# Kernel optimization log

Hardware: AMD Instinct MI355X
Metric: run time of the kernel (lower is better)

## Reference

```python
import math
import jax, jax.numpy as jnp
import numpy as np

HEADS = 8
SCALE_BASE = 512.0
GN_EPS = 1e-5


def _gammas(heads):
    # 1 - exp(linspace(log(1/32), log(1/512), heads))
    return 1.0 - np.exp(np.linspace(math.log(1.0 / 32.0), math.log(1.0 / 512.0), heads))


def _xpos(x, downscale):
    # x: (N, S, d), d even. Faithful to torchscale XPOS with scale_base=512.
    N, S, d = x.shape
    half = d // 2
    scale = (jnp.arange(0, d, 2, dtype=jnp.float32) + 0.4 * d) / (1.4 * d)        # (half,)
    pos = jnp.arange(S, dtype=jnp.float32)
    sc = scale[None, :] ** (pos / SCALE_BASE)[:, None]                             # (S, half)
    inv_freq = 1.0 / (10000.0 ** (jnp.arange(half, dtype=jnp.float32) / half))
    sinusoid = pos[:, None] * inv_freq[None, :]                                    # (S, half)
    sin, cos = jnp.sin(sinusoid), jnp.cos(sinusoid)
    if downscale:
        sc = 1.0 / sc
    # duplicate_interleave == repeat each column twice adjacently
    sin_s = jnp.repeat(sin * sc, 2, axis=-1)                                       # (S, d)
    cos_s = jnp.repeat(cos * sc, 2, axis=-1)
    x1, x2 = x[..., ::2], x[..., 1::2]
    rot = jnp.stack((-x2, x1), axis=-1).reshape(x.shape)                           # rotate_every_two
    return x * cos_s + rot * sin_s


def setup_inputs() -> dict:
    key = jax.random.key(0)
    ks = jax.random.split(key, 6)
    B, S, H = 2, 2048, 1024
    h = HEADS
    d = H // h
    X = jax.random.normal(ks[0], (B, S, H), dtype=jnp.float32)
    # per-head projections, torch init: randn(d, d) / d
    W_Q = jax.random.normal(ks[1], (h, d, d), dtype=jnp.float32) / d
    W_K = jax.random.normal(ks[2], (h, d, d), dtype=jnp.float32) / d
    W_V = jax.random.normal(ks[3], (h, d, d), dtype=jnp.float32) / d
    W_G = jax.random.normal(ks[4], (H, H), dtype=jnp.float32) / H
    W_O = jax.random.normal(ks[5], (H, H), dtype=jnp.float32) / H
    gn_weight = jnp.ones((H,), dtype=jnp.float32)
    gn_bias = jnp.zeros((H,), dtype=jnp.float32)
    return {"X": X, "W_Q": W_Q, "W_K": W_K, "W_V": W_V,
            "W_G": W_G, "W_O": W_O, "gn_weight": gn_weight, "gn_bias": gn_bias}


def reference(X, W_Q, W_K, W_V, W_G, W_O, gn_weight, gn_bias):
    B, S, H = X.shape
    h = HEADS
    d = H // h
    gammas = jnp.asarray(_gammas(h), dtype=X.dtype)                                # (h,)

    Xh = X.reshape(B, S, h, d)
    Q = jnp.einsum('bshd,hde->bhse', Xh, W_Q)                                      # (B,h,S,d)
    K = jnp.einsum('bshd,hde->bhse', Xh, W_K)
    V = jnp.einsum('bshd,hde->bhse', Xh, W_V)

    Q = _xpos(Q.reshape(B * h, S, d), downscale=False).reshape(B, h, S, d)
    K = _xpos(K.reshape(B * h, S, d), downscale=True).reshape(B, h, S, d)

    # decay mask D[h, n, m] = gamma_h^(n-m) for n >= m else 0 (NaN-safe)
    n = jnp.arange(S)
    diff = n[:, None] - n[None, :]                                                 # (S,S)
    causal = (diff >= 0)
    D = (gammas[:, None, None] ** jnp.where(causal, diff, 0).astype(X.dtype)) \
        * causal[None].astype(X.dtype)                                             # (h,S,S)

    att = jnp.einsum('bhsd,bhtd->bhst', Q, K) * D[None]                            # (B,h,S,S)
    Y = jnp.einsum('bhst,bhtd->bshd', att, V).reshape(B, S, H)

    # GroupNorm(heads, hidden) over flattened (B*S, H), biased variance
    Yg = Y.reshape(B * S, h, d)
    mu = Yg.mean(axis=-1, keepdims=True)
    var = Yg.var(axis=-1, keepdims=True)
    Yn = ((Yg - mu) / jnp.sqrt(var + GN_EPS)).reshape(B * S, H)
    Yn = (Yn * gn_weight + gn_bias).reshape(B, S, H)

    G = X @ W_G
    return (G * jax.nn.sigmoid(G) * Yn) @ W_O
```

## Files before the change

kernel.cpp:

```cpp
#include <hip/hip_runtime.h>
#include <math.h>

#define NB 2
#define SEQ 2048
#define HD 1024
#define NH 8
#define DH 128
#define HALF 64

typedef __bf16 bf16_t;
typedef __attribute__((ext_vector_type(8))) __bf16 bf16x8;
typedef __attribute__((ext_vector_type(4))) __bf16 bf16x4;
typedef __attribute__((ext_vector_type(4))) float f32x4;

typedef __attribute__((address_space(1))) void gvoid;
typedef __attribute__((address_space(3))) void lvoid;

__device__ __forceinline__ void gld16(const bf16_t* g, bf16_t* l) {
  __builtin_amdgcn_global_load_lds((gvoid*)g, (lvoid*)l, 16, 0, 0);
}

__device__ __forceinline__ float head_l2g(int hh) {
  double ga = log(1.0/32.0), gbb = log(1.0/512.0);
  float gamma = (float)(1.0 - exp(ga + (double)hh * (gbb - ga) / 7.0));
  return log2f(gamma);
}

__device__ void wsplit_body(const float* __restrict__ in, bf16_t* __restrict__ oh,
                            int M, int N, int bx, int by, int z,
                            float (*tile)[65]) {
  in += (size_t)z * M * N; oh += (size_t)z * M * N;
  int r0 = by * 64, c0 = bx * 64;
  int t = threadIdx.x;
  for (int idx = t; idx < 1024; idx += 256) {
    int r = idx >> 4, c4 = (idx & 15) * 4;
    float4 v = *(const float4*)(in + (size_t)(r0 + r) * N + c0 + c4);
    *(float4*)&tile[r][c4] = v;
  }
  __syncthreads();
  for (int idx = t; idx < 1024; idx += 256) {
    int c = idx >> 4, r4 = (idx & 15) * 4;
    bf16x4 h;
    #pragma unroll
    for (int j = 0; j < 4; ++j)
      h[j] = (bf16_t)tile[r4 + j][c];
    *(bf16x4*)(oh + (size_t)(c0 + c) * M + r0 + r4) = h;
  }
}

__global__ __launch_bounds__(256) void k_prep(
    const float* __restrict__ Wq, const float* __restrict__ Wk,
    const float* __restrict__ Wv, const float* __restrict__ Wg,
    const float* __restrict__ Wo,
    float* __restrict__ tabs, bf16_t* __restrict__ Wqt,
    bf16_t* __restrict__ Wkt, bf16_t* __restrict__ Wvt,
    bf16_t* __restrict__ Wgt, bf16_t* __restrict__ Wot) {
  __shared__ float tile[64][65];
  int b = blockIdx.x;
  if (b < 512) {
    int idx = b * 256 + threadIdx.x;
    int s = idx >> 6, i = idx & 63;
    float dd = (float)DH;
    float scale = (2.0f * (float)i + 0.4f * dd) / (1.4f * dd);
    float sc = expf(logf(scale) * ((float)s / 512.0f));
    float inv_freq = expf(-logf(10000.0f) * ((float)i / (float)HALF));
    float ang = (float)s * inv_freq;
    float sn, cs;
    sincosf(ang, &sn, &cs);
    float rsc = 1.0f / sc;
    tabs[idx]               = sn * sc;
    tabs[SEQ*HALF + idx]    = cs * sc;
    tabs[2*SEQ*HALF + idx]  = sn * rsc;
    tabs[3*SEQ*HALF + idx]  = cs * rsc;
  } else if (b < 608) {
    int i = b - 512;
    int which = i >> 5;
    int j = i & 31;
    const float* in = (which == 0) ? Wq : (which == 1) ? Wk : Wv;
    bf16_t* oh = (which == 0) ? Wqt : (which == 1) ? Wkt : Wvt;
    wsplit_body(in, oh, DH, DH, j & 1, (j >> 1) & 1, j >> 2, tile);
  } else {
    int i = b - 608;
    int which = i >> 8;
    int j = i & 255;
    wsplit_body(which ? Wo : Wg, which ? Wot : Wgt, HD, HD,
                j & 15, j >> 4, 0, tile);
  }
}

__global__ __launch_bounds__(512, 1) void k_qkvd(
    const float* __restrict__ X, const float* __restrict__ tabs,
    const bf16_t* __restrict__ Wqt, const bf16_t* __restrict__ Wkt,
    const bf16_t* __restrict__ Wvt,
    bf16_t* __restrict__ Qo, bf16_t* __restrict__ Ko,
    bf16_t* __restrict__ VTo, bf16_t* __restrict__ Xhg,
    bf16_t* __restrict__ DSt) {
  __shared__ bf16_t Wsh[128][128];
  __shared__ bf16_t KT[128][128];
  __shared__ bf16_t Vd[128][128];
  int t = threadIdx.x;
  int lane = t & 63, w = t >> 6;
  int lr = lane & 15, lg = lane >> 4;
  int c = blockIdx.x, hh = blockIdx.y, b = blockIdx.z;
  int s0 = c * 128;
  size_t bh = (size_t)(b*NH + hh);
  float l2g = head_l2g(hh);

  bf16x8 xh[4];
  {
    const float* xp = X + ((size_t)(b*SEQ + s0 + 16*w + lr)) * HD + hh*DH + 8*lg;
    #pragma unroll
    for (int ks = 0; ks < 4; ++ks) {
      float4 u = *(const float4*)(xp + 32*ks);
      float4 v = *(const float4*)(xp + 32*ks + 4);
      float fv[8] = {u.x,u.y,u.z,u.w,v.x,v.y,v.z,v.w};
      #pragma unroll
      for (int j = 0; j < 8; ++j) xh[ks][j] = (bf16_t)fv[j];
    }
  }
  {
    bf16_t* xo = Xhg + ((size_t)(b*SEQ + s0 + 16*w + lr)) * HD + hh*DH + 8*lg;
    #pragma unroll
    for (int ks = 0; ks < 4; ++ks)
      *(bf16x8*)(xo + 32*ks) = xh[ks];
  }

  const bf16_t* Wp[3] = {Wqt, Wkt, Wvt};

  for (int which = 0; which < 3; ++which) {
    const bf16_t* wp = Wp[which] + (size_t)hh * (DH*DH);
    __syncthreads();
    for (int idx = t; idx < 2048; idx += 512) {
      int e = idx >> 4, kb = idx & 15;
      int kbs = kb ^ (e & 7);
      *(bf16x8*)&Wsh[e][kbs*8] = *(const bf16x8*)(wp + (size_t)e*DH + kb*8);
    }
    __syncthreads();
    f32x4 yacc[8];
    #pragma unroll
    for (int i = 0; i < 8; ++i) yacc[i] = (f32x4){0.f,0.f,0.f,0.f};
    #pragma unroll
    for (int sub = 0; sub < 8; ++sub) {
      int e = 16*sub + lr;
      #pragma unroll
      for (int ks = 0; ks < 4; ++ks) {
        int ch = (lg + 4*ks) ^ (lr & 7);
        bf16x8 bhv = *(const bf16x8*)&Wsh[e][ch*8];
        yacc[sub] = __builtin_amdgcn_mfma_f32_16x16x32_bf16(xh[ks], bhv, yacc[sub], 0, 0, 0);
      }
    }
    if (which < 2) {
      const float* st = tabs + (which ? 2*SEQ*HALF : 0);
      const float* ct = st + SEQ*HALF;
      bf16_t* Op = which ? Ko : Qo;
      #pragma unroll
      for (int sub = 0; sub < 8; ++sub) {
        int e = 16*sub + lr;
        int i = e >> 1;
        #pragma unroll
        for (int reg = 0; reg < 4; ++reg) {
          float v = yacc[sub][reg];
          float p = __shfl_xor(v, 1);
          int tau = 16*w + 4*lg + reg;
          int srow = s0 + tau;
          float sv = st[srow*HALF + i], cv = ct[srow*HALF + i];
          float o = v * cv + ((e & 1) ? p : -p) * sv;
          bf16_t ob = (bf16_t)o;
          Op[(bh*SEQ + srow) * DH + e] = ob;
          if (which == 1) {
            int col = (((tau>>3) ^ (e & 7)) << 3) | (tau & 7);
            KT[e][col] = ob;
          }
        }
      }
    } else {
      float decay[4];
      #pragma unroll
      for (int reg = 0; reg < 4; ++reg)
        decay[reg] = exp2f(l2g * (float)(127 - (16*w + 4*lg + reg)));
      #pragma unroll
      for (int sub = 0; sub < 8; ++sub) {
        int e = 16*sub + lr;
        bf16x4 hv;
        #pragma unroll
        for (int reg = 0; reg < 4; ++reg) {
          int tau = 16*w + 4*lg + reg;
          float f = yacc[sub][reg];
          hv[reg] = (bf16_t)f;
          int col = (((tau>>3) ^ (e & 7)) << 3) | (tau & 7);
          Vd[e][col] = (bf16_t)(f * decay[reg]);
        }
        *(bf16x4*)(VTo + bh * (size_t)(DH*SEQ) + (size_t)e*SEQ + (s0 + 16*w + 4*lg)) = hv;
      }
    }
  }
  __syncthreads();

  f32x4 acc[8];
  #pragma unroll
  for (int s = 0; s < 8; ++s) acc[s] = (f32x4){0.f,0.f,0.f,0.f};
  {
    int dv = 16*w + lr;
    #pragma unroll
    for (int ks = 0; ks < 4; ++ks) {
      int ca = (lg + 4*ks) ^ (dv & 7);
      bf16x8 avh = *(const bf16x8*)&Vd[dv][ca*8];
      #pragma unroll
      for (int sub = 0; sub < 8; ++sub) {
        int dk = 16*sub + lr;
        int cb = (lg + 4*ks) ^ (dk & 7);
        bf16x8 bkh = *(const bf16x8*)&KT[dk][cb*8];
        acc[sub] = __builtin_amdgcn_mfma_f32_16x16x32_bf16(avh, bkh, acc[sub], 0, 0, 0);
      }
    }
  }
  size_t obase = (bh * 16 + c) * 16384;
  #pragma unroll
  for (int sub = 0; sub < 8; ++sub)
    #pragma unroll
    for (int reg = 0; reg < 4; ++reg) {
      int dv = 16*w + 4*lg + reg;
      int dk = 16*sub + lr;
      DSt[obase + (size_t)dv*128 + dk] = (bf16_t)acc[sub][reg];
    }
}

__global__ __launch_bounds__(256) void k_scan(bf16_t* __restrict__ DSt) {
  int t = threadIdx.x;
  int bh = blockIdx.y, hh = bh & 7;
  float l2g = head_l2g(hh);
  float g128 = exp2f(l2g * 128.0f);
  int dv = blockIdx.x * 16 + (t >> 4);
  int dk0 = (t & 15) * 8;
  size_t base = ((size_t)bh * 16) * 16384 + (size_t)dv*128 + dk0;
  float S[8] = {};
  for (int c = 0; c < 16; ++c) {
    size_t off = base + (size_t)c * 16384;
    bf16x8 dh = *(const bf16x8*)(DSt + off);
    bf16x8 sh;
    #pragma unroll
    for (int j = 0; j < 8; ++j) sh[j] = (bf16_t)S[j];
    *(bf16x8*)(DSt + off) = sh;
    #pragma unroll
    for (int j = 0; j < 8; ++j)
      S[j] = g128*S[j] + (float)dh[j];
  }
}

__global__ __launch_bounds__(512, 1) void k_ret(
    const bf16_t* __restrict__ Qg, const bf16_t* __restrict__ Kg,
    const bf16_t* __restrict__ VTg, const bf16_t* __restrict__ DSt,
    const float* __restrict__ gw, const float* __restrict__ gb,
    bf16_t* __restrict__ Yn) {
  __shared__ bf16_t Ksh[64][128];
  __shared__ bf16_t Vsh[128][64];
  __shared__ bf16_t Ph[128][64];
  int t = threadIdx.x;
  int lane = t & 63, w = t >> 6;
  int lr = lane & 15, lg = lane >> 4;
  int c = blockIdx.x, bh = blockIdx.y, hh = bh & 7;
  int s0 = c * 128;
  size_t base  = (size_t)bh * SEQ * DH;
  size_t vbase = (size_t)bh * DH * SEQ;
  float l2g = head_l2g(hh);
  float colf = exp2f(-l2g * (float)lr);
  float g16v[4];
  #pragma unroll
  for (int ts = 0; ts < 4; ++ts) g16v[ts] = exp2f(-l2g * (float)(16*ts));

  bf16x8 qh[4];
  {
    const bf16_t* qp = Qg + base + (size_t)(s0 + 16*w + lr) * DH + lg * 8;
    #pragma unroll
    for (int ks = 0; ks < 4; ++ks)
      qh[ks] = *(const bf16x8*)(qp + 32*ks);
  }
  f32x4 yacc[8];
  #pragma unroll
  for (int i = 0; i < 8; ++i) yacc[i] = (f32x4){0.f,0.f,0.f,0.f};

  for (int idx = t; idx < 1024; idx += 512) {
    int r = idx >> 4, kb = idx & 15;
    int kbs = kb ^ (r & 7);
    *(bf16x8*)&Ksh[r][kbs*8] = *(const bf16x8*)(Kg + base + (size_t)(s0 + r)*DH + kb*8);
  }
  for (int idx = t; idx < 1024; idx += 512) {
    int d = idx >> 3, cb = idx & 7;
    int cbs = cb ^ (d & 7);
    *(bf16x8*)&Vsh[d][cbs*8] = *(const bf16x8*)(VTg + vbase + (size_t)d*SEQ + s0 + cb*8);
  }

  {
    const bf16_t* sth = DSt + ((size_t)bh * 16 + c) * 16384;
    #pragma unroll
    for (int sub = 0; sub < 8; ++sub) {
      size_t ro = (size_t)(16*sub + lr) * 128 + 8*lg;
      #pragma unroll
      for (int ks = 0; ks < 4; ++ks) {
        bf16x8 bh_ = *(const bf16x8*)(sth + ro + 32*ks);
        yacc[sub] = __builtin_amdgcn_mfma_f32_16x16x32_bf16(qh[ks], bh_, yacc[sub], 0, 0, 0);
      }
    }
    float rowc[4];
    #pragma unroll
    for (int reg = 0; reg < 4; ++reg)
      rowc[reg] = exp2f(l2g * (float)(16*w + 4*lg + reg + 1));
    #pragma unroll
    for (int sub = 0; sub < 8; ++sub)
      #pragma unroll
      for (int reg = 0; reg < 4; ++reg)
        yacc[sub][reg] *= rowc[reg];
  }
  __syncthreads();

  for (int kt = 0; kt < 2; ++kt) {
    int t0 = kt * 64;
    if (kt == 1) {
      __syncthreads();
      for (int idx = t; idx < 1024; idx += 512) {
        int r = idx >> 4, kb = idx & 15;
        int kbs = kb ^ (r & 7);
        *(bf16x8*)&Ksh[r][kbs*8] = *(const bf16x8*)(Kg + base + (size_t)(s0 + 64 + r)*DH + kb*8);
      }
      for (int idx = t; idx < 1024; idx += 512) {
        int d = idx >> 3, cb = idx & 7;
        int cbs = cb ^ (d & 7);
        *(bf16x8*)&Vsh[d][cbs*8] = *(const bf16x8*)(VTg + vbase + (size_t)d*SEQ + s0 + 64 + cb*8);
      }
    }
    __syncthreads();
    if (!(kt == 1 && w < 4)) {
      float rowf[4];
      #pragma unroll
      for (int reg = 0; reg < 4; ++reg)
        rowf[reg] = exp2f(l2g * (float)(16*w + 4*lg + reg - t0));

      #pragma unroll
      for (int ts = 0; ts < 4; ++ts) {
        f32x4 sacc = (f32x4){0.f,0.f,0.f,0.f};
        int trow = 16*ts + lr;
        #pragma unroll
        for (int ks = 0; ks < 4; ++ks) {
          int kbs = (4*ks + lg) ^ (trow & 7);
          bf16x8 kh8 = *(const bf16x8*)&Ksh[trow][kbs*8];
          sacc = __builtin_amdgcn_mfma_f32_16x16x32_bf16(qh[ks], kh8, sacc, 0, 0, 0);
        }
        float cf = colf * g16v[ts];
        #pragma unroll
        for (int reg = 0; reg < 4; ++reg) {
          int qloc = 4*lg + reg;
          int diff = (16*w + qloc) - (t0 + trow);
          float p = (diff >= 0) ? sacc[reg] * (rowf[reg] * cf) : 0.0f;
          int cb = (trow >> 3) ^ (qloc & 7);
          Ph[16*w + qloc][cb*8 + (trow & 7)] = (bf16_t)p;
        }
      }
      #pragma unroll
      for (int ks = 0; ks < 2; ++ks) {
        int prow = 16*w + lr;
        int pcb = (4*ks + lg) ^ (lr & 7);
        bf16x8 pah = *(const bf16x8*)&Ph[prow][pcb*8];
        #pragma unroll
        for (int sub = 0; sub < 8; ++sub) {
          int drow = 16*sub + lr;
          int vcb = (4*ks + lg) ^ (drow & 7);
          bf16x8 vh8 = *(const bf16x8*)&Vsh[drow][vcb*8];
          yacc[sub] = __builtin_amdgcn_mfma_f32_16x16x32_bf16(pah, vh8, yacc[sub], 0, 0, 0);
        }
      }
    }
  }

  float s1v[4] = {0.f,0.f,0.f,0.f}, s2v[4] = {0.f,0.f,0.f,0.f};
  #pragma unroll
  for (int sub = 0; sub < 8; ++sub)
    #pragma unroll
    for (int reg = 0; reg < 4; ++reg) {
      float v = yacc[sub][reg];
      s1v[reg] += v;
      s2v[reg] += v * v;
    }
  #pragma unroll
  for (int off = 8; off; off >>= 1)
    #pragma unroll
    for (int reg = 0; reg < 4; ++reg) {
      s1v[reg] += __shfl_xor(s1v[reg], off);
      s2v[reg] += __shfl_xor(s2v[reg], off);
    }
  float gwv[8], gbv[8];
  #pragma unroll
  for (int sub = 0; sub < 8; ++sub) {
    gwv[sub] = gw[hh*DH + 16*sub + lr];
    gbv[sub] = gb[hh*DH + 16*sub + lr];
  }
  int b = bh >> 3;
  #pragma unroll
  for (int reg = 0; reg < 4; ++reg) {
    float mean = s1v[reg] * (1.0f/128.0f);
    float var = s2v[reg] * (1.0f/128.0f) - mean*mean;
    float inv = rsqrtf(var + 1e-5f);
    int srow = s0 + 16*w + 4*lg + reg;
    bf16_t* op = Yn + (size_t)(b*SEQ + srow) * HD + hh*DH;
    #pragma unroll
    for (int sub = 0; sub < 8; ++sub)
      op[16*sub + lr] = (bf16_t)((yacc[sub][reg] - mean) * inv * gwv[sub] + gbv[sub]);
  }
}

__global__ __launch_bounds__(256, 2) void k_gemm(
    const bf16_t* __restrict__ Ag, const bf16_t* __restrict__ Bg,
    const bf16_t* __restrict__ E,
    bf16_t* __restrict__ Oh, float* __restrict__ Of, int mode) {
  __shared__ bf16_t SA[2][64][64];
  __shared__ bf16_t SBB[2][128][64];
  int t = threadIdx.x;
  int lane = t & 63, w = t >> 6;
  int lr = lane & 15, lg = lane >> 4;
  int wr = w >> 1, wc = w & 1;
  int bid = blockIdx.x;
  int xcd = bid & 7, local = bid >> 3;
  int mp = xcd * 8 + (local >> 3);
  int np = local & 7;
  int m0 = mp * 64, n0 = np * 128;

  const bf16_t* As = Ag + (size_t)m0 * HD;
  const bf16_t* Bs = Bg + (size_t)n0 * HD;

  f32x4 acc[2][4];
  #pragma unroll
  for (int i = 0; i < 2; ++i)
    #pragma unroll
    for (int j = 0; j < 4; ++j) acc[i][j] = (f32x4){0.f,0.f,0.f,0.f};

  int srow = lane >> 3, sch = lane & 7;

  {
    #pragma unroll
    for (int i = 0; i < 2; ++i) {
      int row = w*16 + i*8 + srow;
      int kc = (sch ^ (row & 7)) * 8;
      gld16(As + (size_t)row*HD + kc, &SA[0][w*16 + i*8][0]);
    }
    #pragma unroll
    for (int i = 0; i < 4; ++i) {
      int row = w*32 + i*8 + srow;
      int kc = (sch ^ (row & 7)) * 8;
      gld16(Bs + (size_t)row*HD + kc, &SBB[0][w*32 + i*8][0]);
    }
  }
  __syncthreads();

  int buf = 0;
  for (int kt = 0; kt < 16; ++kt) {
    if (kt + 1 < 16) {
      int k0 = (kt + 1) * 64;
      #pragma unroll
      for (int i = 0; i < 2; ++i) {
        int row = w*16 + i*8 + srow;
        int kc = (sch ^ (row & 7)) * 8;
        gld16(As + (size_t)row*HD + k0 + kc, &SA[buf^1][w*16 + i*8][0]);
      }
      #pragma unroll
      for (int i = 0; i < 4; ++i) {
        int row = w*32 + i*8 + srow;
        int kc = (sch ^ (row & 7)) * 8;
        gld16(Bs + (size_t)row*HD + k0 + kc, &SBB[buf^1][w*32 + i*8][0]);
      }
    }
    #pragma unroll
    for (int ks = 0; ks < 2; ++ks) {
      bf16x8 a_[2], b_[4];
      #pragma unroll
      for (int mf = 0; mf < 2; ++mf) {
        int row = wr*32 + mf*16 + lr;
        int ch = (lg + 4*ks) ^ (row & 7);
        a_[mf] = *(const bf16x8*)&SA[buf][row][ch*8];
      }
      #pragma unroll
      for (int nf = 0; nf < 4; ++nf) {
        int row = wc*64 + nf*16 + lr;
        int ch = (lg + 4*ks) ^ (row & 7);
        b_[nf] = *(const bf16x8*)&SBB[buf][row][ch*8];
      }
      #pragma unroll
      for (int mf = 0; mf < 2; ++mf)
        #pragma unroll
        for (int nf = 0; nf < 4; ++nf)
          acc[mf][nf] = __builtin_amdgcn_mfma_f32_16x16x32_bf16(a_[mf], b_[nf], acc[mf][nf], 0, 0, 0);
    }
    __syncthreads();
    buf ^= 1;
  }
  #pragma unroll
  for (int mf = 0; mf < 2; ++mf) {
    #pragma unroll
    for (int nf = 0; nf < 4; ++nf) {
      #pragma unroll
      for (int reg = 0; reg < 4; ++reg) {
        int m = m0 + wr*32 + mf*16 + 4*lg + reg;
        int n = n0 + wc*64 + nf*16 + lr;
        float g = acc[mf][nf][reg];
        size_t off = (size_t)m * HD + n;
        if (mode == 1) {
          float sg = 1.0f / (1.0f + expf(-g));
          Oh[off] = (bf16_t)(g * sg * (float)E[off]);
        } else {
          Of[off] = g;
        }
      }
    }
  }
}

extern "C" void kernel_launch(void* const* d_in, const int* in_sizes, int n_in,
                              void* d_out, int out_size, void* d_ws, size_t ws_size,
                              hipStream_t stream) {
  const float* X  = (const float*)d_in[0];
  const float* Wq = (const float*)d_in[1];
  const float* Wk = (const float*)d_in[2];
  const float* Wv = (const float*)d_in[3];
  const float* Wg = (const float*)d_in[4];
  const float* Wo = (const float*)d_in[5];
  const float* gw = (const float*)d_in[6];
  const float* gb = (const float*)d_in[7];
  float* out = (float*)d_out;
  float* ws = (float*)d_ws;

  float* tabs = ws;
  bf16_t* Q   = (bf16_t*)(ws + 524288);
  bf16_t* K   = Q + 4194304;
  bf16_t* VT  = K + 4194304;
  bf16_t* Yn  = VT + 4194304;
  bf16_t* DSt = Yn + 4194304;
  bf16_t* Wqt = DSt + 4194304;
  bf16_t* Wkt = Wqt + 131072;
  bf16_t* Wvt = Wkt + 131072;
  bf16_t* Wgt = Wvt + 131072;
  bf16_t* Wot = Wgt + 1048576;
  bf16_t* Xh  = Wot + 1048576;
  bf16_t* A2  = Q;

  k_prep<<<dim3(1120), dim3(256), 0, stream>>>(Wq, Wk, Wv, Wg, Wo, tabs,
                                               Wqt, Wkt, Wvt, Wgt, Wot);
  k_qkvd<<<dim3(16, 8, 2), dim3(512), 0, stream>>>(X, tabs, Wqt, Wkt, Wvt,
                                                   Q, K, VT, Xh, DSt);
  k_scan<<<dim3(8, 16), dim3(256), 0, stream>>>(DSt);
  k_ret<<<dim3(16, 16), dim3(512), 0, stream>>>(Q, K, VT, DSt, gw, gb, Yn);
  k_gemm<<<dim3(512), dim3(256), 0, stream>>>(Xh, Wgt, Yn, A2, nullptr, 1);
  k_gemm<<<dim3(512), dim3(256), 0, stream>>>(A2, Wot, nullptr, nullptr, out, 0);
}
```

Baseline: 98.10 us.

## Fuse chunk-state scan into retention kernel and move big weight transposes there

Removes the separate k_scan launch: each retention block now recomputes its own prefix state by summing the decayed chunk states of all preceding chunks and stages it in LDS. The W_G/W_O transpose-to-bf16 work moves from k_prep into extra blocks of the retention launch, so it can overlap with retention work. K/V/W tile loads switch to direct global-to-LDS loads. The cost is redundant prefix work (up to 15 chunk reads per block), which is uneven across blocks, plus more LDS per block.

```diff
diff --git a/kernel.cpp b/kernel.cpp
--- a/kernel.cpp
+++ b/kernel.cpp
@@ -26,19 +26,18 @@
   return log2f(gamma);
 }
 
-__device__ void wsplit_body(const float* __restrict__ in, bf16_t* __restrict__ oh,
-                            int M, int N, int bx, int by, int z,
-                            float (*tile)[65]) {
+__device__ __forceinline__ void wsplit_body(
+    const float* in, bf16_t* oh, int M, int N,
+    int bx, int by, int z, float (*tile)[65], int nthr, int t) {
   in += (size_t)z * M * N; oh += (size_t)z * M * N;
   int r0 = by * 64, c0 = bx * 64;
-  int t = threadIdx.x;
-  for (int idx = t; idx < 1024; idx += 256) {
+  for (int idx = t; idx < 1024; idx += nthr) {
     int r = idx >> 4, c4 = (idx & 15) * 4;
     float4 v = *(const float4*)(in + (size_t)(r0 + r) * N + c0 + c4);
     *(float4*)&tile[r][c4] = v;
   }
   __syncthreads();
-  for (int idx = t; idx < 1024; idx += 256) {
+  for (int idx = t; idx < 1024; idx += nthr) {
     int c = idx >> 4, r4 = (idx & 15) * 4;
     bf16x4 h;
     #pragma unroll
@@ -50,11 +49,9 @@
 
 __global__ __launch_bounds__(256) void k_prep(
     const float* __restrict__ Wq, const float* __restrict__ Wk,
-    const float* __restrict__ Wv, const float* __restrict__ Wg,
-    const float* __restrict__ Wo,
+    const float* __restrict__ Wv,
     float* __restrict__ tabs, bf16_t* __restrict__ Wqt,
-    bf16_t* __restrict__ Wkt, bf16_t* __restrict__ Wvt,
-    bf16_t* __restrict__ Wgt, bf16_t* __restrict__ Wot) {
+    bf16_t* __restrict__ Wkt, bf16_t* __restrict__ Wvt) {
   __shared__ float tile[64][65];
   int b = blockIdx.x;
   if (b < 512) {
@@ -72,19 +69,14 @@
     tabs[SEQ*HALF + idx]    = cs * sc;
     tabs[2*SEQ*HALF + idx]  = sn * rsc;
     tabs[3*SEQ*HALF + idx]  = cs * rsc;
-  } else if (b < 608) {
+  } else {
     int i = b - 512;
     int which = i >> 5;
     int j = i & 31;
     const float* in = (which == 0) ? Wq : (which == 1) ? Wk : Wv;
     bf16_t* oh = (which == 0) ? Wqt : (which == 1) ? Wkt : Wvt;
-    wsplit_body(in, oh, DH, DH, j & 1, (j >> 1) & 1, j >> 2, tile);
-  } else {
-    int i = b - 608;
-    int which = i >> 8;
-    int j = i & 255;
-    wsplit_body(which ? Wo : Wg, which ? Wot : Wgt, HD, HD,
-                j & 15, j >> 4, 0, tile);
+    wsplit_body(in, oh, DH, DH, j & 1, (j >> 1) & 1, j >> 2, tile,
+                256, threadIdx.x);
   }
 }
 
@@ -130,10 +122,11 @@
   for (int which = 0; which < 3; ++which) {
     const bf16_t* wp = Wp[which] + (size_t)hh * (DH*DH);
     __syncthreads();
-    for (int idx = t; idx < 2048; idx += 512) {
-      int e = idx >> 4, kb = idx & 15;
-      int kbs = kb ^ (e & 7);
-      *(bf16x8*)&Wsh[e][kbs*8] = *(const bf16x8*)(wp + (size_t)e*DH + kb*8);
+    #pragma unroll
+    for (int i = 0; i < 4; ++i) {
+      int e = w*16 + i*4 + (lane >> 4);
+      int kb = (lane & 15) ^ (e & 7);
+      gld16(wp + (size_t)e*DH + kb*8, &Wsh[w*16 + i*4][0]);
     }
     __syncthreads();
     f32x4 yacc[8];
@@ -225,40 +218,31 @@
     }
 }
 
-__global__ __launch_bounds__(256) void k_scan(bf16_t* __restrict__ DSt) {
-  int t = threadIdx.x;
-  int bh = blockIdx.y, hh = bh & 7;
-  float l2g = head_l2g(hh);
-  float g128 = exp2f(l2g * 128.0f);
-  int dv = blockIdx.x * 16 + (t >> 4);
-  int dk0 = (t & 15) * 8;
-  size_t base = ((size_t)bh * 16) * 16384 + (size_t)dv*128 + dk0;
-  float S[8] = {};
-  for (int c = 0; c < 16; ++c) {
-    size_t off = base + (size_t)c * 16384;
-    bf16x8 dh = *(const bf16x8*)(DSt + off);
-    bf16x8 sh;
-    #pragma unroll
-    for (int j = 0; j < 8; ++j) sh[j] = (bf16_t)S[j];
-    *(bf16x8*)(DSt + off) = sh;
-    #pragma unroll
-    for (int j = 0; j < 8; ++j)
-      S[j] = g128*S[j] + (float)dh[j];
-  }
-}
-
 __global__ __launch_bounds__(512, 1) void k_ret(
     const bf16_t* __restrict__ Qg, const bf16_t* __restrict__ Kg,
     const bf16_t* __restrict__ VTg, const bf16_t* __restrict__ DSt,
     const float* __restrict__ gw, const float* __restrict__ gb,
-    bf16_t* __restrict__ Yn) {
+    bf16_t* __restrict__ Yn,
+    const float* __restrict__ Wg, const float* __restrict__ Wo,
+    bf16_t* __restrict__ Wgt, bf16_t* __restrict__ Wot) {
   __shared__ bf16_t Ksh[64][128];
   __shared__ bf16_t Vsh[128][64];
   __shared__ bf16_t Ph[128][64];
+  __shared__ bf16_t Slds[128][128];
+  __shared__ float tile[64][65];
   int t = threadIdx.x;
+  int bid = blockIdx.x;
+  if (bid >= 256) {
+    int i = bid - 256;
+    int which = i >> 8;
+    int j = i & 255;
+    wsplit_body(which ? Wo : Wg, which ? Wot : Wgt, HD, HD,
+                j & 15, j >> 4, 0, tile, 512, t);
+    return;
+  }
   int lane = t & 63, w = t >> 6;
   int lr = lane & 15, lg = lane >> 4;
-  int c = blockIdx.x, bh = blockIdx.y, hh = bh & 7;
+  int c = bid & 15, bh = bid >> 4, hh = bh & 7;
   int s0 = c * 128;
   size_t base  = (size_t)bh * SEQ * DH;
   size_t vbase = (size_t)bh * DH * SEQ;
@@ -268,6 +252,19 @@
   #pragma unroll
   for (int ts = 0; ts < 4; ++ts) g16v[ts] = exp2f(-l2g * (float)(16*ts));
 
+  #pragma unroll
+  for (int i = 0; i < 2; ++i) {
+    int r = w*8 + i*4 + (lane >> 4);
+    int kb = (lane & 15) ^ (r & 7);
+    gld16(Kg + base + (size_t)(s0 + r)*DH + kb*8, &Ksh[w*8 + i*4][0]);
+  }
+  #pragma unroll
+  for (int i = 0; i < 2; ++i) {
+    int d = w*16 + i*8 + (lane >> 3);
+    int cb = (lane & 7) ^ (d & 7);
+    gld16(VTg + vbase + (size_t)d*SEQ + s0 + cb*8, &Vsh[w*16 + i*8][0]);
+  }
+
   bf16x8 qh[4];
   {
     const bf16_t* qp = Qg + base + (size_t)(s0 + 16*w + lr) * DH + lg * 8;
@@ -275,30 +272,51 @@
     for (int ks = 0; ks < 4; ++ks)
       qh[ks] = *(const bf16x8*)(qp + 32*ks);
   }
+
+  {
+    float g128 = exp2f(l2g * 128.0f);
+    float S0[8] = {}, S1[8] = {}, S2[8] = {}, S3[8] = {};
+    const bf16_t* dbase = DSt + ((size_t)bh * 16) * 16384
+                        + (size_t)(t >> 2) * 128 + (t & 3) * 32;
+    for (int cp = 0; cp < c; ++cp) {
+      const bf16_t* dp = dbase + (size_t)cp * 16384;
+      bf16x8 d0 = *(const bf16x8*)dp;
+      bf16x8 d1 = *(const bf16x8*)(dp + 8);
+      bf16x8 d2 = *(const bf16x8*)(dp + 16);
+      bf16x8 d3 = *(const bf16x8*)(dp + 24);
+      #pragma unroll
+      for (int j = 0; j < 8; ++j) {
+        S0[j] = g128*S0[j] + (float)d0[j];
+        S1[j] = g128*S1[j] + (float)d1[j];
+        S2[j] = g128*S2[j] + (float)d2[j];
+        S3[j] = g128*S3[j] + (float)d3[j];
+      }
+    }
+    int dv = t >> 2;
+    #pragma unroll
+    for (int q = 0; q < 4; ++q) {
+      const float* Sq = (q == 0) ? S0 : (q == 1) ? S1 : (q == 2) ? S2 : S3;
+      int ch = ((t & 3) * 4 + q) ^ (dv & 7);
+      bf16x8 s8;
+      #pragma unroll
+      for (int j = 0; j < 8; ++j) s8[j] = (bf16_t)Sq[j];
+      *(bf16x8*)&Slds[dv][ch*8] = s8;
+    }
+  }
+  __syncthreads();
+
   f32x4 yacc[8];
   #pragma unroll
   for (int i = 0; i < 8; ++i) yacc[i] = (f32x4){0.f,0.f,0.f,0.f};
-
-  for (int idx = t; idx < 1024; idx += 512) {
-    int r = idx >> 4, kb = idx & 15;
-    int kbs = kb ^ (r & 7);
-    *(bf16x8*)&Ksh[r][kbs*8] = *(const bf16x8*)(Kg + base + (size_t)(s0 + r)*DH + kb*8);
-  }
-  for (int idx = t; idx < 1024; idx += 512) {
-    int d = idx >> 3, cb = idx & 7;
-    int cbs = cb ^ (d & 7);
-    *(bf16x8*)&Vsh[d][cbs*8] = *(const bf16x8*)(VTg + vbase + (size_t)d*SEQ + s0 + cb*8);
-  }
-
-  {
-    const bf16_t* sth = DSt + ((size_t)bh * 16 + c) * 16384;
+  {
     #pragma unroll
     for (int sub = 0; sub < 8; ++sub) {
-      size_t ro = (size_t)(16*sub + lr) * 128 + 8*lg;
+      int dv = 16*sub + lr;
       #pragma unroll
       for (int ks = 0; ks < 4; ++ks) {
-        bf16x8 bh_ = *(const bf16x8*)(sth + ro + 32*ks);
-        yacc[sub] = __builtin_amdgcn_mfma_f32_16x16x32_bf16(qh[ks], bh_, yacc[sub], 0, 0, 0);
+        int ch = (lg + 4*ks) ^ (dv & 7);
+        bf16x8 b8 = *(const bf16x8*)&Slds[dv][ch*8];
+        yacc[sub] = __builtin_amdgcn_mfma_f32_16x16x32_bf16(qh[ks], b8, yacc[sub], 0, 0, 0);
       }
     }
     float rowc[4];
@@ -311,24 +329,25 @@
       for (int reg = 0; reg < 4; ++reg)
         yacc[sub][reg] *= rowc[reg];
   }
-  __syncthreads();
 
   for (int kt = 0; kt < 2; ++kt) {
     int t0 = kt * 64;
     if (kt == 1) {
       __syncthreads();
-      for (int idx = t; idx < 1024; idx += 512) {
-        int r = idx >> 4, kb = idx & 15;
-        int kbs = kb ^ (r & 7);
-        *(bf16x8*)&Ksh[r][kbs*8] = *(const bf16x8*)(Kg + base + (size_t)(s0 + 64 + r)*DH + kb*8);
-      }
-      for (int idx = t; idx < 1024; idx += 512) {
-        int d = idx >> 3, cb = idx & 7;
-        int cbs = cb ^ (d & 7);
-        *(bf16x8*)&Vsh[d][cbs*8] = *(const bf16x8*)(VTg + vbase + (size_t)d*SEQ + s0 + 64 + cb*8);
-      }
-    }
-    __syncthreads();
+      #pragma unroll
+      for (int i = 0; i < 2; ++i) {
+        int r = w*8 + i*4 + (lane >> 4);
+        int kb = (lane & 15) ^ (r & 7);
+        gld16(Kg + base + (size_t)(s0 + 64 + r)*DH + kb*8, &Ksh[w*8 + i*4][0]);
+      }
+      #pragma unroll
+      for (int i = 0; i < 2; ++i) {
+        int d = w*16 + i*8 + (lane >> 3);
+        int cb = (lane & 7) ^ (d & 7);
+        gld16(VTg + vbase + (size_t)d*SEQ + s0 + 64 + cb*8, &Vsh[w*16 + i*8][0]);
+      }
+      __syncthreads();
+    }
     if (!(kt == 1 && w < 4)) {
       float rowf[4];
       #pragma unroll
@@ -540,12 +559,11 @@
   bf16_t* Xh  = Wot + 1048576;
   bf16_t* A2  = Q;
 
-  k_prep<<<dim3(1120), dim3(256), 0, stream>>>(Wq, Wk, Wv, Wg, Wo, tabs,
-                                               Wqt, Wkt, Wvt, Wgt, Wot);
+  k_prep<<<dim3(608), dim3(256), 0, stream>>>(Wq, Wk, Wv, tabs, Wqt, Wkt, Wvt);
   k_qkvd<<<dim3(16, 8, 2), dim3(512), 0, stream>>>(X, tabs, Wqt, Wkt, Wvt,
                                                    Q, K, VT, Xh, DSt);
-  k_scan<<<dim3(8, 16), dim3(256), 0, stream>>>(DSt);
-  k_ret<<<dim3(16, 16), dim3(512), 0, stream>>>(Q, K, VT, DSt, gw, gb, Yn);
+  k_ret<<<dim3(768), dim3(512), 0, stream>>>(Q, K, VT, DSt, gw, gb, Yn,
+                                             Wg, Wo, Wgt, Wot);
   k_gemm<<<dim3(512), dim3(256), 0, stream>>>(Xh, Wgt, Yn, A2, nullptr, 1);
   k_gemm<<<dim3(512), dim3(256), 0, stream>>>(A2, Wot, nullptr, nullptr, out, 0);
 }
```

New measurement: 95.49 us. 1.03x faster.
